# Kernel tuning notes

Measured on AMD Instinct MI355X. Metric: run time of the kernel, lower is better.

## Reference

```python
import jax, jax.numpy as jnp
import numpy as np

EPS = 1e-4  # self.epsilon

@jax.custom_vjp
def heavi_tanh(x):
    # forward: hard heaviside H(x) = 0 for x<=0 else 1
    return jnp.where(x <= 0.0, 0.0, 1.0).astype(x.dtype)

def _heavi_fwd(x):
    return heavi_tanh(x), x

def _heavi_bwd(x, dy):
    # surrogate gradient: d/dx [0.5 + 0.5*tanh(k*x)] with k=1 -> 1 - tanh(x)^2
    return (dy * (1.0 - jnp.tanh(x) ** 2),)

heavi_tanh.defvjp(_heavi_fwd, _heavi_bwd)

def setup_inputs() -> dict:
    key = jax.random.key(0)
    k1, k2, k3 = jax.random.split(key, 3)
    B, D = 2048, 3706
    return {
        "fake_tensor": jax.random.uniform(k1, (B, D), dtype=jnp.float32),
        "min_boundary_value": jax.random.uniform(k2, (D,), dtype=jnp.float32),
        "interval_lengths": jax.random.uniform(k3, (D, 4), dtype=jnp.float32),
    }

def reference(fake_tensor, min_boundary_value, interval_lengths):
    # boundary values: b[:,0]=min_boundary, b[:,i]=b[:,i-1]+relu(len[:,i-1])+eps  -> cumsum
    steps = jax.nn.relu(interval_lengths) + EPS                      # [D,4]
    b = jnp.cumsum(jnp.concatenate([min_boundary_value[:, None], steps], axis=1), axis=1)  # [D,5]

    r = jnp.arange(6.0, dtype=fake_tensor.dtype)                     # target ratings 0..5
    k = jnp.arange(5.0, dtype=fake_tensor.dtype)                     # boundary idx 0..4
    s = jnp.sign(r[:, None] - k[None, :] - 0.5)                      # [6,5] constant sign matrix

    p2 = fake_tensor[:, :, None] - b[None, :, :]                     # [B,D,5] a - b_jk
    x = s[None, None, :, :] * p2[:, :, None, :]                      # [B,D,6,5]
    dist = jnp.prod(heavi_tanh(x), axis=-1)                          # [B,D,6]
    val = dist @ r                                                   # [B,D]
    return dist, val
```

## Files before the change

kernel.cpp:

```cpp
#include <hip/hip_runtime.h>

#define EPS 1e-4f

constexpr int B = 2048;
constexpr int D = 3706;
constexpr int NP = B * D / 2;

__device__ __forceinline__ void bucketize(float a, float mb, float4 L,
                                          float* __restrict__ r6, float& v) {
    const float s0 = fmaxf(L.x, 0.0f) + EPS;
    const float s1 = fmaxf(L.y, 0.0f) + EPS;
    const float s2 = fmaxf(L.z, 0.0f) + EPS;
    const float s3 = fmaxf(L.w, 0.0f) + EPS;
    const float b0 = mb;
    const float b1 = b0 + s0;
    const float b2 = b1 + s1;
    const float b3 = b2 + s2;
    const float b4 = b3 + s3;

    const int cnt = (int)(a > b0) + (int)(a > b1) + (int)(a > b2)
                  + (int)(a > b3) + (int)(a > b4);
    const bool eq = (a == b0) | (a == b1) | (a == b2) | (a == b3) | (a == b4);
    const float ok = eq ? 0.0f : 1.0f;

#pragma unroll
    for (int r = 0; r < 6; ++r) r6[r] = (r == cnt) ? ok : 0.0f;
    v = eq ? 0.0f : (float)cnt;
}

__global__ __launch_bounds__(256) void disc_kernel(
        const float* __restrict__ fake,
        const float* __restrict__ minb,
        const float* __restrict__ lens,
        float* __restrict__ out) {
    const int p = blockIdx.x * 256 + threadIdx.x;
    if (p >= NP) return;
    const int flat = p << 1;
    const int d0 = flat % D;

    const float2 a2 = reinterpret_cast<const float2*>(fake)[p];
    const float2 mb = *reinterpret_cast<const float2*>(minb + d0);
    const float4 L0 = reinterpret_cast<const float4*>(lens)[d0];
    const float4 L1 = reinterpret_cast<const float4*>(lens)[d0 + 1];

    float r0[6], r1[6], v0, v1;
    bucketize(a2.x, mb.x, L0, r0, v0);
    bucketize(a2.y, mb.y, L1, r1, v1);

    float4* dp = reinterpret_cast<float4*>(out + (size_t)flat * 6);
    dp[0] = make_float4(r0[0], r0[1], r0[2], r0[3]);
    dp[1] = make_float4(r0[4], r0[5], r1[0], r1[1]);
    dp[2] = make_float4(r1[2], r1[3], r1[4], r1[5]);

    float* val = out + (size_t)B * D * 6;
    reinterpret_cast<float2*>(val)[p] = make_float2(v0, v1);
}

extern "C" void kernel_launch(void* const* d_in, const int* in_sizes, int n_in,
                              void* d_out, int out_size, void* d_ws, size_t ws_size,
                              hipStream_t stream) {
    const float* fake = (const float*)d_in[0];
    const float* minb = (const float*)d_in[1];
    const float* lens = (const float*)d_in[2];
    float* out = (float*)d_out;

    const int grid = (NP + 255) / 256;
    disc_kernel<<<grid, 256, 0, stream>>>(fake, minb, lens, out);
}
```

Before: 260.2 us.

## Assign one output float4 per thread for fully coalesced stores

```diff
diff --git a/kernel.cpp b/kernel.cpp
--- a/kernel.cpp
+++ b/kernel.cpp
@@ -4,10 +4,14 @@
 
 constexpr int B = 2048;
 constexpr int D = 3706;
-constexpr int NP = B * D / 2;
+constexpr unsigned BD = (unsigned)B * (unsigned)D;
+constexpr unsigned K4 = BD * 6u / 4u;
+constexpr unsigned V4 = BD / 4u;
+constexpr unsigned NT = K4 + V4;
+constexpr int BLOCK = 256;
 
-__device__ __forceinline__ void bucketize(float a, float mb, float4 L,
-                                          float* __restrict__ r6, float& v) {
+__device__ __forceinline__ void bucketize(const float a, const float mb, const float4 L,
+                                          int& cnt, float& ok) {
     const float s0 = fmaxf(L.x, 0.0f) + EPS;
     const float s1 = fmaxf(L.y, 0.0f) + EPS;
     const float s2 = fmaxf(L.z, 0.0f) + EPS;
@@ -17,43 +21,65 @@
     const float b2 = b1 + s1;
     const float b3 = b2 + s2;
     const float b4 = b3 + s3;
-
-    const int cnt = (int)(a > b0) + (int)(a > b1) + (int)(a > b2)
-                  + (int)(a > b3) + (int)(a > b4);
+    cnt = (int)(a > b0) + (int)(a > b1) + (int)(a > b2)
+        + (int)(a > b3) + (int)(a > b4);
     const bool eq = (a == b0) | (a == b1) | (a == b2) | (a == b3) | (a == b4);
-    const float ok = eq ? 0.0f : 1.0f;
-
-#pragma unroll
-    for (int r = 0; r < 6; ++r) r6[r] = (r == cnt) ? ok : 0.0f;
-    v = eq ? 0.0f : (float)cnt;
+    ok = eq ? 0.0f : 1.0f;
 }
 
-__global__ __launch_bounds__(256) void disc_kernel(
+__global__ __launch_bounds__(BLOCK) void disc_kernel(
         const float* __restrict__ fake,
         const float* __restrict__ minb,
         const float* __restrict__ lens,
         float* __restrict__ out) {
-    const int p = blockIdx.x * 256 + threadIdx.x;
-    if (p >= NP) return;
-    const int flat = p << 1;
-    const int d0 = flat % D;
+    const unsigned id = blockIdx.x * BLOCK + threadIdx.x;
 
-    const float2 a2 = reinterpret_cast<const float2*>(fake)[p];
-    const float2 mb = *reinterpret_cast<const float2*>(minb + d0);
-    const float4 L0 = reinterpret_cast<const float4*>(lens)[d0];
-    const float4 L1 = reinterpret_cast<const float4*>(lens)[d0 + 1];
+    if (id < K4) {
+        const unsigned m  = id;
+        const unsigned e0 = (4u * m) / 6u;
+        const unsigned e1 = (4u * m + 3u) / 6u;
 
-    float r0[6], r1[6], v0, v1;
-    bucketize(a2.x, mb.x, L0, r0, v0);
-    bucketize(a2.y, mb.y, L1, r1, v1);
+        const unsigned d0 = e0 % (unsigned)D;
+        int c0; float k0;
+        bucketize(fake[e0], minb[d0],
+                  reinterpret_cast<const float4*>(lens)[d0], c0, k0);
 
-    float4* dp = reinterpret_cast<float4*>(out + (size_t)flat * 6);
-    dp[0] = make_float4(r0[0], r0[1], r0[2], r0[3]);
-    dp[1] = make_float4(r0[4], r0[5], r1[0], r1[1]);
-    dp[2] = make_float4(r1[2], r1[3], r1[4], r1[5]);
+        const unsigned d1 = e1 % (unsigned)D;
+        int c1; float k1;
+        bucketize(fake[e1], minb[d1],
+                  reinterpret_cast<const float4*>(lens)[d1], c1, k1);
 
-    float* val = out + (size_t)B * D * 6;
-    reinterpret_cast<float2*>(val)[p] = make_float2(v0, v1);
+        float4 f;
+        float* fp = &f.x;
+        const unsigned base = 4u * m;
+#pragma unroll
+        for (int j = 0; j < 4; ++j) {
+            const unsigned g    = base + (unsigned)j;
+            const unsigned e    = g / 6u;
+            const unsigned slot = g - 6u * e;
+            const int   cc = (e == e0) ? c0 : c1;
+            const float kk = (e == e0) ? k0 : k1;
+            fp[j] = ((int)slot == cc) ? kk : 0.0f;
+        }
+        reinterpret_cast<float4*>(out)[m] = f;
+    } else {
+        const unsigned v = id - K4;
+        const unsigned e = 4u * v;
+        const float4 a4 = reinterpret_cast<const float4*>(fake)[v];
+        const float* ap = &a4.x;
+        float4 f;
+        float* fp = &f.x;
+#pragma unroll
+        for (int j = 0; j < 4; ++j) {
+            const unsigned ej = e + (unsigned)j;
+            const unsigned dj = ej % (unsigned)D;
+            int c; float k;
+            bucketize(ap[j], minb[dj],
+                      reinterpret_cast<const float4*>(lens)[dj], c, k);
+            fp[j] = k * (float)c;
+        }
+        reinterpret_cast<float4*>(out + (size_t)BD * 6u)[v] = f;
+    }
 }
 
 extern "C" void kernel_launch(void* const* d_in, const int* in_sizes, int n_in,
@@ -64,6 +90,6 @@
     const float* lens = (const float*)d_in[2];
     float* out = (float*)d_out;
 
-    const int grid = (NP + 255) / 256;
-    disc_kernel<<<grid, 256, 0, stream>>>(fake, minb, lens, out);
+    const unsigned grid = NT / (unsigned)BLOCK;
+    disc_kernel<<<grid, BLOCK, 0, stream>>>(fake, minb, lens, out);
 }
```

New measurement: 273.3 us. +5.0%, slower.
